# Optimization experiments

Hardware: AMD Instinct MI355X
Metric: run time of the kernel (lower is better)

## Reference

```python
import jax, jax.numpy as jnp
import numpy as np

QMAX = 7.0  # 4-bit symmetric: levels in [-8, 7]

def quant4(w):
    # per-tensor symmetric 4-bit fake-quant with straight-through estimator
    s = jnp.max(jnp.abs(w)) / QMAX
    q = jnp.clip(jnp.round(w / s), -8.0, 7.0) * s
    return w + jax.lax.stop_gradient(q - w)

def setup_inputs() -> dict:
    key = jax.random.key(0)
    ks = jax.random.split(key, 7)
    B = 2048
    x = jax.random.normal(ks[0], (B, 1, 31, 16, 31), dtype=jnp.float32)
    # conv: out_ch=1, in_ch=1, kernel (5,3,5)
    w_conv = jax.random.normal(ks[1], (1, 1, 5, 3, 5), dtype=jnp.float32) * 0.1
    b_conv = jax.random.normal(ks[2], (1,), dtype=jnp.float32) * 0.1
    w_fc1 = jax.random.normal(ks[3], (128, 343), dtype=jnp.float32) * 0.05
    b_fc1 = jax.random.normal(ks[4], (128,), dtype=jnp.float32) * 0.05
    w_fc2 = jax.random.normal(ks[5], (4, 128), dtype=jnp.float32) * 0.05
    b_fc2 = jax.random.normal(ks[6], (4,), dtype=jnp.float32) * 0.05
    return {"x": x, "w_conv": w_conv, "b_conv": b_conv,
            "w_fc1": w_fc1, "b_fc1": b_fc1, "w_fc2": w_fc2, "b_fc2": b_fc2}

def reference(x, w_conv, b_conv, w_fc1, b_fc1, w_fc2, b_fc2):
    # QuantConv3d: 4-bit quantized weights, stride (2,1,2), no padding
    c1 = jax.lax.conv_general_dilated(
        x, quant4(w_conv), window_strides=(2, 1, 2), padding='VALID',
        dimension_numbers=('NCDHW', 'OIDHW', 'NCDHW'))
    c1 = c1 + b_conv.reshape(1, -1, 1, 1, 1)          # [B,1,14,14,14]
    # MaxPool3d(2)
    p1 = jax.lax.reduce_window(c1, -jnp.inf, jax.lax.max,
                               (1, 1, 2, 2, 2), (1, 1, 2, 2, 2), 'VALID')  # [B,1,7,7,7]
    f = p1.reshape(p1.shape[0], -1)                   # [B,343]
    a1 = jax.nn.relu(f @ quant4(w_fc1).T + b_fc1)     # [B,128]
    s2 = a1 @ quant4(w_fc2).T + b_fc2                 # [B,4]
    return jax.nn.softmax(s2, axis=1)
```

## Files before the change

### kernel.cpp

```cpp
#include <hip/hip_runtime.h>
#include <hip/hip_bf16.h>

#define WS_WCONV   128
#define WS_W1T     256
#define WS_W2      44160

__device__ __forceinline__ float q4(float w, float s) {
  if (s <= 0.f) return 0.f;
  float r = rintf(w / s);
  r = fminf(fmaxf(r, -8.f), 7.f);
  return r * s;
}

__global__ __launch_bounds__(256) void quant_all(
    const float* __restrict__ wconv, const float* __restrict__ w1,
    const float* __restrict__ w2, float* __restrict__ ws) {
  __shared__ float red[256];
  int b = blockIdx.x, t = threadIdx.x;
  if (b < 88) {
    const float4* w4 = (const float4*)w1;
    float m = 0.f;
    for (int i = t; i < 10976; i += 256) {
      float4 v = w4[i];
      m = fmaxf(m, fmaxf(fmaxf(fabsf(v.x), fabsf(v.y)),
                         fmaxf(fabsf(v.z), fabsf(v.w))));
    }
    red[t] = m;
    __syncthreads();
    for (int s = 128; s > 0; s >>= 1) {
      if (t < s) red[t] = fmaxf(red[t], red[t + s]);
      __syncthreads();
    }
    float s = red[0] * (1.0f / 7.0f);
    #pragma unroll
    for (int k = 0; k < 2; ++k) {
      int idx = b * 512 + k * 256 + t;
      if (idx < 43904) {
        float q = q4(w1[idx], s);
        int o = idx / 343;
        int j = idx - o * 343;
        ws[WS_W1T + j * 128 + o] = q;
      }
    }
  } else {
    float mc = (t < 75) ? fabsf(wconv[t]) : 0.f;
    float m2 = 0.f;
    for (int i = t; i < 512; i += 256) m2 = fmaxf(m2, fabsf(w2[i]));
    red[t] = mc;
    __syncthreads();
    for (int s = 128; s > 0; s >>= 1) {
      if (t < s) red[t] = fmaxf(red[t], red[t + s]);
      __syncthreads();
    }
    float sc = red[0] * (1.0f / 7.0f);
    __syncthreads();
    red[t] = m2;
    __syncthreads();
    for (int s = 128; s > 0; s >>= 1) {
      if (t < s) red[t] = fmaxf(red[t], red[t + s]);
      __syncthreads();
    }
    float s2 = red[0] * (1.0f / 7.0f);
    if (t < 75) ws[WS_WCONV + t] = q4(wconv[t], sc);
    #pragma unroll
    for (int k = 0; k < 2; ++k) {
      int idx = k * 256 + t;
      ws[WS_W2 + idx] = q4(w2[idx], s2);
    }
  }
}

__device__ __forceinline__ void conv_phase(
    const float* __restrict__ xs, const float* __restrict__ wq,
    int t, int npf, int pd_off, float bc, float* __restrict__ feat) {
  if (t >= npf) return;
  int pdl = t / 49;
  int rr  = t - pdl * 49;
  int ph  = rr / 7;
  int pw  = rr - ph * 7;
  float c[2][2][2];
  #pragma unroll
  for (int i = 0; i < 8; ++i) ((float*)c)[i] = 0.f;
  int base0 = pdl * 1984 + ph * 62 + pw * 4;
  #pragma unroll
  for (int dd = 0; dd < 7; ++dd) {
    int rbase = base0 + dd * 496;
    #pragma unroll
    for (int hh = 0; hh < 4; ++hh) {
      float row[7];
      #pragma unroll
      for (int wi = 0; wi < 7; ++wi) row[wi] = xs[rbase + hh * 31 + wi];
      #pragma unroll
      for (int odp = 0; odp < 2; ++odp) {
        int kd = dd - 2 * odp;
        if (kd < 0 || kd > 4) continue;
        #pragma unroll
        for (int ohp = 0; ohp < 2; ++ohp) {
          int kh = hh - ohp;
          if (kh < 0 || kh > 2) continue;
          #pragma unroll
          for (int owp = 0; owp < 2; ++owp) {
            float a = c[odp][ohp][owp];
            #pragma unroll
            for (int kw = 0; kw < 5; ++kw)
              a = fmaf(row[2 * owp + kw], wq[kd * 15 + kh * 5 + kw], a);
            c[odp][ohp][owp] = a;
          }
        }
      }
    }
  }
  float m = ((float*)c)[0];
  #pragma unroll
  for (int i = 1; i < 8; ++i) m = fmaxf(m, ((float*)c)[i]);
  feat[(pdl + pd_off) * 49 + rr] = m + bc;
}

__global__ __launch_bounds__(256, 4) void fused_net(
    const float* __restrict__ x, const float* __restrict__ bconv,
    const float* __restrict__ ws, const float* __restrict__ bfc1,
    const float* __restrict__ bfc2, float* __restrict__ out) {
  __shared__ float xs[9424];
  __shared__ float feat[344];
  __shared__ float fc1p[128];
  __shared__ float a1[128];
  __shared__ float s2[4];
  int t = threadIdx.x;
  int b = blockIdx.x;
  const float* wq = ws + WS_WCONV;
  float bc = bconv[0];

  {
    const float4* src = (const float4*)(x + (size_t)b * 15376);
    float4* dst = (float4*)xs;
    for (int i = t; i < 2356; i += 256) dst[i] = src[i];
    if (t == 0) feat[343] = 0.f;
  }
  __syncthreads();
  conv_phase(xs, wq, t, 196, 0, bc, feat);
  __syncthreads();
  {
    const float4* src = (const float4*)(x + (size_t)b * 15376 + 16 * 496);
    float4* dst = (float4*)xs;
    for (int i = t; i < 1860; i += 256) dst[i] = src[i];
  }
  __syncthreads();
  conv_phase(xs, wq, t, 147, 4, bc, feat);
  __syncthreads();

  int g = t >> 7, o = t & 127;
  {
    const float* w1T = ws + WS_W1T;
    int j0 = g ? 172 : 0;
    const float4* f4 = (const float4*)&feat[j0];
    const float* wp = w1T + j0 * 128 + o;
    float p0 = 0.f, p1 = 0.f, p2 = 0.f, p3 = 0.f;
    for (int q = 0; q < 43; ++q) {
      float4 ff = f4[q];
      p0 = fmaf(ff.x, wp[0],   p0);
      p1 = fmaf(ff.y, wp[128], p1);
      p2 = fmaf(ff.z, wp[256], p2);
      p3 = fmaf(ff.w, wp[384], p3);
      wp += 512;
    }
    float acc = (p0 + p1) + (p2 + p3);
    if (g) fc1p[o] = acc;
    __syncthreads();
    if (!g) a1[o] = fmaxf(acc + fc1p[o] + bfc1[o], 0.f);
  }
  __syncthreads();

  if (t < 64) {
    int cls = t & 3, kk = t >> 2;
    const float* w2 = ws + WS_W2 + cls * 128 + kk * 8;
    const float* av = a1 + kk * 8;
    float p = 0.f;
    #pragma unroll
    for (int i = 0; i < 8; ++i) p = fmaf(av[i], w2[i], p);
    p += __shfl_down(p, 32);
    p += __shfl_down(p, 16);
    p += __shfl_down(p, 8);
    p += __shfl_down(p, 4);
    if (t < 4) s2[t] = p + bfc2[t];
  }
  __syncthreads();
  if (t < 4) {
    float v0 = s2[0], v1 = s2[1], v2 = s2[2], v3 = s2[3];
    float m = fmaxf(fmaxf(v0, v1), fmaxf(v2, v3));
    float e0 = expf(v0 - m), e1 = expf(v1 - m);
    float e2 = expf(v2 - m), e3 = expf(v3 - m);
    float inv = 1.f / (e0 + e1 + e2 + e3);
    float mine = (t == 0) ? e0 : (t == 1) ? e1 : (t == 2) ? e2 : e3;
    out[b * 4 + t] = mine * inv;
  }
}

extern "C" void kernel_launch(void* const* d_in, const int* in_sizes, int n_in,
                              void* d_out, int out_size, void* d_ws, size_t ws_size,
                              hipStream_t stream) {
  const float* x     = (const float*)d_in[0];
  const float* wconv = (const float*)d_in[1];
  const float* bconv = (const float*)d_in[2];
  const float* wfc1  = (const float*)d_in[3];
  const float* bfc1  = (const float*)d_in[4];
  const float* wfc2  = (const float*)d_in[5];
  const float* bfc2  = (const float*)d_in[6];
  float* out = (float*)d_out;
  float* ws  = (float*)d_ws;

  quant_all<<<89, 256, 0, stream>>>(wconv, wfc1, wfc2, ws);
  fused_net<<<2048, 256, 0, stream>>>(x, bconv, ws, bfc1, bfc2, out);
}
```

Measured before the change: 225.7 us.

## Stage input rows padded to 32 with XOR swizzle for float4 LDS reads

```diff
diff --git a/kernel.cpp b/kernel.cpp
--- a/kernel.cpp
+++ b/kernel.cpp
@@ -70,6 +70,21 @@
   }
 }
 
+__device__ __forceinline__ void stage_chunk(
+    const float* __restrict__ x, int b, int d0, int ndep,
+    float* __restrict__ xs, int t) {
+  int ntask = ndep * 16 * 8;
+  for (int i = t; i < ntask; i += 256) {
+    int r = i >> 3, q = i & 7;
+    int d = r >> 4, h = r & 15;
+    const float* g = x + (size_t)b * 15376 + (d0 + d) * 496 + h * 31 + 4 * q;
+    float v0 = g[0], v1 = g[1], v2 = g[2];
+    float v3 = (q < 7) ? g[3] : 0.f;
+    int dst = d * 512 + h * 32 + ((q ^ (h & 7)) << 2);
+    *(float4*)&xs[dst] = make_float4(v0, v1, v2, v3);
+  }
+}
+
 __device__ __forceinline__ void conv_phase(
     const float* __restrict__ xs, const float* __restrict__ wq,
     int t, int npf, int pd_off, float bc, float* __restrict__ feat) {
@@ -81,15 +96,17 @@
   float c[2][2][2];
   #pragma unroll
   for (int i = 0; i < 8; ++i) ((float*)c)[i] = 0.f;
-  int base0 = pdl * 1984 + ph * 62 + pw * 4;
   #pragma unroll
   for (int dd = 0; dd < 7; ++dd) {
-    int rbase = base0 + dd * 496;
+    int dbase = (4 * pdl + dd) * 512;
     #pragma unroll
     for (int hh = 0; hh < 4; ++hh) {
-      float row[7];
-      #pragma unroll
-      for (int wi = 0; wi < 7; ++wi) row[wi] = xs[rbase + hh * 31 + wi];
+      int h = 2 * ph + hh;
+      int hb = h & 7;
+      int base = dbase + h * 32;
+      float4 ra = *(const float4*)&xs[base + (((pw)     ^ hb) << 2)];
+      float4 rb = *(const float4*)&xs[base + (((pw + 1) ^ hb) << 2)];
+      float row[8] = {ra.x, ra.y, ra.z, ra.w, rb.x, rb.y, rb.z, rb.w};
       #pragma unroll
       for (int odp = 0; odp < 2; ++odp) {
         int kd = dd - 2 * odp;
@@ -120,32 +137,24 @@
     const float* __restrict__ x, const float* __restrict__ bconv,
     const float* __restrict__ ws, const float* __restrict__ bfc1,
     const float* __restrict__ bfc2, float* __restrict__ out) {
-  __shared__ float xs[9424];
+  __shared__ float xs[9728];
   __shared__ float feat[344];
-  __shared__ float fc1p[128];
-  __shared__ float a1[128];
-  __shared__ float s2[4];
+  float* fc1p = xs;
+  float* a1   = xs + 128;
+  float* s2   = xs + 256;
   int t = threadIdx.x;
   int b = blockIdx.x;
   const float* wq = ws + WS_WCONV;
   float bc = bconv[0];
 
-  {
-    const float4* src = (const float4*)(x + (size_t)b * 15376);
-    float4* dst = (float4*)xs;
-    for (int i = t; i < 2356; i += 256) dst[i] = src[i];
-    if (t == 0) feat[343] = 0.f;
-  }
-  __syncthreads();
-  conv_phase(xs, wq, t, 196, 0, bc, feat);
-  __syncthreads();
-  {
-    const float4* src = (const float4*)(x + (size_t)b * 15376 + 16 * 496);
-    float4* dst = (float4*)xs;
-    for (int i = t; i < 1860; i += 256) dst[i] = src[i];
-  }
-  __syncthreads();
-  conv_phase(xs, wq, t, 147, 4, bc, feat);
+  if (t == 0) feat[343] = 0.f;
+  stage_chunk(x, b, 0, 15, xs, t);
+  __syncthreads();
+  conv_phase(xs, wq, t, 147, 0, bc, feat);
+  __syncthreads();
+  stage_chunk(x, b, 12, 19, xs, t);
+  __syncthreads();
+  conv_phase(xs, wq, t, 196, 3, bc, feat);
   __syncthreads();
 
   int g = t >> 7, o = t & 127;
```

New measurement: 228.4 us. No clear change (+1.2%).

## Stage input in four smaller depth chunks to raise occupancy; vectorize fc1 weights

Applied to the files above, without the earlier changes.

```diff
diff --git a/kernel.cpp b/kernel.cpp
--- a/kernel.cpp
+++ b/kernel.cpp
@@ -2,8 +2,8 @@
 #include <hip/hip_bf16.h>
 
 #define WS_WCONV   128
-#define WS_W1T     256
-#define WS_W2      44160
+#define WS_W1B     256
+#define WS_W2      44288
 
 __device__ __forceinline__ float q4(float w, float s) {
   if (s <= 0.f) return 0.f;
@@ -39,7 +39,7 @@
         float q = q4(w1[idx], s);
         int o = idx / 343;
         int j = idx - o * 343;
-        ws[WS_W1T + j * 128 + o] = q;
+        ws[WS_W1B + (j >> 2) * 512 + 4 * o + (j & 3)] = q;
       }
     }
   } else {
@@ -68,6 +68,15 @@
       ws[WS_W2 + idx] = q4(w2[idx], s2);
     }
   }
+}
+
+__device__ __forceinline__ void stage(
+    const float* __restrict__ x, int b, int d0, int ndep,
+    float* __restrict__ xs, int t) {
+  const float4* src = (const float4*)(x + (size_t)b * 15376 + d0 * 496);
+  float4* dst = (float4*)xs;
+  int n = ndep * 124;
+  for (int i = t; i < n; i += 256) dst[i] = src[i];
 }
 
 __device__ __forceinline__ void conv_phase(
@@ -116,52 +125,46 @@
   feat[(pdl + pd_off) * 49 + rr] = m + bc;
 }
 
-__global__ __launch_bounds__(256, 4) void fused_net(
+__global__ __launch_bounds__(256, 6) void fused_net(
     const float* __restrict__ x, const float* __restrict__ bconv,
     const float* __restrict__ ws, const float* __restrict__ bfc1,
     const float* __restrict__ bfc2, float* __restrict__ out) {
-  __shared__ float xs[9424];
+  __shared__ float xs[5456];
   __shared__ float feat[344];
-  __shared__ float fc1p[128];
-  __shared__ float a1[128];
-  __shared__ float s2[4];
+  float* fc1p = xs;
+  float* a1   = xs + 128;
+  float* s2   = xs + 256;
   int t = threadIdx.x;
   int b = blockIdx.x;
   const float* wq = ws + WS_WCONV;
   float bc = bconv[0];
 
-  {
-    const float4* src = (const float4*)(x + (size_t)b * 15376);
-    float4* dst = (float4*)xs;
-    for (int i = t; i < 2356; i += 256) dst[i] = src[i];
-    if (t == 0) feat[343] = 0.f;
-  }
-  __syncthreads();
-  conv_phase(xs, wq, t, 196, 0, bc, feat);
-  __syncthreads();
-  {
-    const float4* src = (const float4*)(x + (size_t)b * 15376 + 16 * 496);
-    float4* dst = (float4*)xs;
-    for (int i = t; i < 1860; i += 256) dst[i] = src[i];
-  }
-  __syncthreads();
-  conv_phase(xs, wq, t, 147, 4, bc, feat);
-  __syncthreads();
+  if (t == 0) feat[343] = 0.f;
+  int par = b & 1;
+  #pragma unroll
+  for (int ci = 0; ci < 4; ++ci) {
+    int c = par ? (3 - ci) : ci;
+    int d0 = 8 * c;
+    int ndep = (c == 3) ? 7 : 11;
+    stage(x, b, d0, ndep, xs, t);
+    __syncthreads();
+    conv_phase(xs, wq, t, (c == 3) ? 49 : 98, 2 * c, bc, feat);
+    __syncthreads();
+  }
 
   int g = t >> 7, o = t & 127;
   {
-    const float* w1T = ws + WS_W1T;
-    int j0 = g ? 172 : 0;
-    const float4* f4 = (const float4*)&feat[j0];
-    const float* wp = w1T + j0 * 128 + o;
+    const float* w1b = ws + WS_W1B;
+    int q0 = g ? 43 : 0;
+    const float4* f4 = (const float4*)feat;
     float p0 = 0.f, p1 = 0.f, p2 = 0.f, p3 = 0.f;
-    for (int q = 0; q < 43; ++q) {
-      float4 ff = f4[q];
-      p0 = fmaf(ff.x, wp[0],   p0);
-      p1 = fmaf(ff.y, wp[128], p1);
-      p2 = fmaf(ff.z, wp[256], p2);
-      p3 = fmaf(ff.w, wp[384], p3);
-      wp += 512;
+    for (int q = q0; q < q0 + 43; ++q) {
+      float4 f = f4[q];
+      float4 w = *(const float4*)&w1b[q * 512 + 4 * o];
+      p0 = fmaf(f.x, w.x, p0);
+      p1 = fmaf(f.y, w.y, p1);
+      p2 = fmaf(f.z, w.z, p2);
+      p3 = fmaf(f.w, w.w, p3);
     }
     float acc = (p0 + p1) + (p2 + p3);
     if (g) fc1p[o] = acc;
@@ -172,11 +175,14 @@
 
   if (t < 64) {
     int cls = t & 3, kk = t >> 2;
-    const float* w2 = ws + WS_W2 + cls * 128 + kk * 8;
-    const float* av = a1 + kk * 8;
+    const float4* w2 = (const float4*)(ws + WS_W2 + cls * 128 + kk * 8);
+    const float4* av = (const float4*)(a1 + kk * 8);
+    float4 aa = av[0], ab = av[1], wa = w2[0], wb = w2[1];
     float p = 0.f;
-    #pragma unroll
-    for (int i = 0; i < 8; ++i) p = fmaf(av[i], w2[i], p);
+    p = fmaf(aa.x, wa.x, p); p = fmaf(aa.y, wa.y, p);
+    p = fmaf(aa.z, wa.z, p); p = fmaf(aa.w, wa.w, p);
+    p = fmaf(ab.x, wb.x, p); p = fmaf(ab.y, wb.y, p);
+    p = fmaf(ab.z, wb.z, p); p = fmaf(ab.w, wb.w, p);
     p += __shfl_down(p, 32);
     p += __shfl_down(p, 16);
     p += __shfl_down(p, 8);
```

Result: slower. 230.3 us (+2.1%).
